# Performance work log

Hardware: AMD Instinct MI355X
Metric: run time of the kernel (lower is better)

The kernel has to match this reference:

```python
import jax, jax.numpy as jnp
import numpy as np

NHEAD, TOKEN_DIM, HIDDEN, OUT_DIM = 4, 768, 256, 768
B, L = 16, 1024
EPS = 1e-5
SLOPE = 0.01  # default LeakyReLU negative_slope


def _layernorm(x, g, b):
    mu = jnp.mean(x, axis=-1, keepdims=True)
    var = jnp.var(x, axis=-1, keepdims=True)
    return (x - mu) * jax.lax.rsqrt(var + EPS) * g + b


def setup_inputs() -> dict:
    key = jax.random.key(0)
    ks = jax.random.split(key, 8)
    s = 0.02
    return {
        "token_embedding": jax.random.normal(ks[0], (B, L, TOKEN_DIM), jnp.float32),
        "W_fc": jax.random.normal(ks[1], (NHEAD, TOKEN_DIM, HIDDEN), jnp.float32) * s,
        "b_fc": jnp.zeros((NHEAD, HIDDEN), jnp.float32),
        "ln_g": jnp.ones((NHEAD, HIDDEN), jnp.float32),
        "ln_b": jnp.zeros((NHEAD, HIDDEN), jnp.float32),
        "a_w": jax.random.normal(ks[2], (NHEAD, 2 * HIDDEN), jnp.float32) * s,
        "a_b": jnp.zeros((NHEAD,), jnp.float32),
        "W_cat": jax.random.normal(ks[3], (NHEAD * HIDDEN, OUT_DIM), jnp.float32) * s,
        "b_cat": jnp.zeros((OUT_DIM,), jnp.float32),
        "lnO_g": jnp.ones((OUT_DIM,), jnp.float32),
        "lnO_b": jnp.zeros((OUT_DIM,), jnp.float32),
        "W_fcs": jax.random.normal(ks[4], (3, OUT_DIM, OUT_DIM), jnp.float32) * s,
        "b_fcs": jnp.zeros((3, OUT_DIM), jnp.float32),
    }


def reference(token_embedding, W_fc, b_fc, ln_g, ln_b, a_w, a_b,
              W_cat, b_cat, lnO_g, lnO_b, W_fcs, b_fcs):
    # per-head projection + layernorm: h [n, B, L, H]
    h = jnp.einsum('bld,ndh->nblh', token_embedding, W_fc) + b_fc[:, None, None, :]
    h = _layernorm(h, ln_g[:, None, None, :], ln_b[:, None, None, :])
    # attn_fc(concat[h_j, h_i]) decomposes linearly:
    # score[n,b,i,j] = a1 . h[n,b,j] + a2 . h[n,b,i] + bias
    s_row = jnp.einsum('nblh,nh->nbl', h, a_w[:, :HIDDEN])   # varies with j
    s_col = jnp.einsum('nblh,nh->nbl', h, a_w[:, HIDDEN:])   # varies with i
    e = s_col[:, :, :, None] + s_row[:, :, None, :] + a_b[:, None, None, None]
    e = jnp.where(e >= 0, e, SLOPE * e)  # LeakyReLU
    attn = jax.nn.softmax(e, axis=-1)    # softmax over j
    h_prime = jnp.einsum('nbij,nbjh->nbih', attn, h)  # [n, B, L, H]
    # concat heads on feature dim -> [B, L, n*H]
    concat_out = jnp.transpose(h_prime, (1, 2, 0, 3)).reshape(B, L, NHEAD * HIDDEN)
    sent = jnp.mean(concat_out, axis=1)  # [B, n*H]
    sent = sent @ W_cat + b_cat
    sent = _layernorm(sent, lnO_g, lnO_b)
    dims_out = [sent @ W_fcs[i] + b_fcs[i] for i in range(3)]
    return (dims_out[0], dims_out[1], dims_out[2], sent)
```

## Files before the change

kernel.cpp:

```cpp
#include <hip/hip_runtime.h>
#include <math.h>


#define NH   4
#define TD   768
#define HID  256
#define OD   768
#define BB   16
#define LL   1024
#define RTOT (BB*LL)
#define L2E  1.4426950408889634f

typedef __attribute__((ext_vector_type(8))) short bf16x8;
typedef __attribute__((ext_vector_type(4))) float f32x4;

#if __has_builtin(__builtin_amdgcn_exp2f)
#define EXP2(x) __builtin_amdgcn_exp2f(x)
#else
#define EXP2(x) __expf((x) * 0.6931471805599453f)
#endif
#if __has_builtin(__builtin_amdgcn_logf)
#define LOG2(x) __builtin_amdgcn_logf(x)
#else
#define LOG2(x) (__logf(x) * L2E)
#endif

__device__ __forceinline__ float lrelu(float x) { return fmaxf(x, 0.01f * x); }

__device__ __forceinline__ float waveReduceSum(float v) {
  #pragma unroll
  for (int m = 1; m < 64; m <<= 1) v += __shfl_xor(v, m, 64);
  return v;
}
__device__ __forceinline__ float waveReduceMax(float v) {
  #pragma unroll
  for (int m = 1; m < 64; m <<= 1) v = fmaxf(v, __shfl_xor(v, m, 64));
  return v;
}
__device__ __forceinline__ float red16(float v) {
  v += __shfl_xor(v, 1, 64); v += __shfl_xor(v, 2, 64);
  v += __shfl_xor(v, 4, 64); v += __shfl_xor(v, 8, 64);
  return v;
}

__device__ __forceinline__ unsigned short f2b(float f) {
  union { float f; unsigned u; } v; v.f = f;
  unsigned u = v.u;
  return (unsigned short)((u + 0x7fffu + ((u >> 16) & 1u)) >> 16);
}
__device__ __forceinline__ float b2f(unsigned short h) {
  union { unsigned u; float f; } v; v.u = ((unsigned)h) << 16;
  return v.f;
}

__device__ __forceinline__ void gll16(const void* g, void* l) {
  __builtin_amdgcn_global_load_lds(
      (const __attribute__((address_space(1))) unsigned int*)g,
      (__attribute__((address_space(3))) unsigned int*)l, 16, 0, 0);
}

__global__ __launch_bounds__(256) void kconv(const float* __restrict__ T,
                                             const float* __restrict__ Wfc,
                                             unsigned short* __restrict__ Tb,
                                             unsigned short* __restrict__ Wtb) {
  __shared__ float tile[64][65];
  const int t = threadIdx.x;
  if (blockIdx.x < 6144) {
    const size_t i = ((size_t)blockIdx.x * 256 + t) * 8;
    const float4 a = *(const float4*)(T + i);
    const float4 b = *(const float4*)(T + i + 4);
    bf16x8 o;
    o[0] = (short)f2b(a.x); o[1] = (short)f2b(a.y);
    o[2] = (short)f2b(a.z); o[3] = (short)f2b(a.w);
    o[4] = (short)f2b(b.x); o[5] = (short)f2b(b.y);
    o[6] = (short)f2b(b.z); o[7] = (short)f2b(b.w);
    *(bf16x8*)(Tb + i) = o;
  } else {
    const int b2 = blockIdx.x - 6144;
    const int ct = b2 & 3;
    const int kt = (b2 >> 2) % 12;
    const int n  = b2 / 48;
    #pragma unroll
    for (int i = 0; i < 16; ++i) {
      const int kl = i * 4 + (t >> 6), cl = t & 63;
      tile[kl][cl] =
          Wfc[(size_t)n * TD * HID + (size_t)(kt * 64 + kl) * HID + ct * 64 + cl];
    }
    __syncthreads();
    #pragma unroll
    for (int i = 0; i < 16; ++i) {
      const int cl = i * 4 + (t >> 6), kl = t & 63;
      Wtb[(size_t)n * HID * TD + (size_t)(ct * 64 + cl) * TD + kt * 64 + kl] =
          f2b(tile[kl][cl]);
    }
  }
}

__global__ __launch_bounds__(512) void k1_mfma(
    const unsigned short* __restrict__ Tb,
    const unsigned short* __restrict__ Wtb,
    const float* __restrict__ bfc, const float* __restrict__ lng,
    const float* __restrict__ lnb, const float* __restrict__ aw,
    unsigned short* __restrict__ hb,
    float* __restrict__ sR, float* __restrict__ sC)
{
  const int n    = blockIdx.x >> 6;
  const int mb   = blockIdx.x & 63;
  const int t    = threadIdx.x;
  const int lane = t & 63;
  const int wq   = __builtin_amdgcn_readfirstlane(t >> 6);
  const int wm   = wq >> 1;
  const int wn   = wq & 1;
  const int cl   = lane & 15;
  const int rg   = lane >> 4;
  const int row0 = mb * 256;

  __shared__ __align__(16) char smem[131072];

  f32x4 acc[4][8];
  #pragma unroll
  for (int mi = 0; mi < 4; ++mi)
    #pragma unroll
    for (int ni = 0; ni < 8; ++ni) acc[mi][ni] = (f32x4){0.f, 0.f, 0.f, 0.f};

  const char* Tg = (const char*)Tb;
  const char* Wg = (const char*)(Wtb + (size_t)n * HID * TD);

  #define STAGE(buf, k0)                                                       \
    do {                                                                       \
      char* base_ = smem + (buf) * 65536;                                      \
      _Pragma("unroll")                                                        \
      for (int i_ = 0; i_ < 4; ++i_) {                                         \
        const int off_ = i_ * 8192 + t * 16;                                   \
        const int r_ = off_ >> 7, kb_ = off_ & 127;                            \
        const int kbs_ = kb_ ^ ((r_ & 7) << 4);                                \
        gll16(Tg + ((size_t)(row0 + r_) * TD + (k0)) * 2 + kbs_, base_ + off_);\
      }                                                                        \
      _Pragma("unroll")                                                        \
      for (int i_ = 0; i_ < 4; ++i_) {                                         \
        const int off_ = i_ * 8192 + t * 16;                                   \
        const int c_ = off_ >> 7, kb_ = off_ & 127;                            \
        const int kbs_ = kb_ ^ ((c_ & 7) << 4);                                \
        gll16(Wg + ((size_t)c_ * TD + (k0)) * 2 + kbs_, base_ + 32768 + off_); \
      }                                                                        \
    } while (0)

  STAGE(0, 0);
  __syncthreads();
  int cur = 0;
  for (int kt = 0; kt < 12; ++kt) {
    if (kt < 11) STAGE(cur ^ 1, (kt + 1) * 64);
    const char* As = smem + cur * 65536;
    const char* Bs = As + 32768;
    #pragma unroll
    for (int ks = 0; ks < 64; ks += 32) {
      bf16x8 av[4], bv[8];
      const int kk2 = (ks + rg * 8) * 2;
      #pragma unroll
      for (int mi = 0; mi < 4; ++mi) {
        const int row = wm * 64 + mi * 16 + cl;
        av[mi] = *(const bf16x8*)(As + row * 128 + (kk2 ^ ((row & 7) << 4)));
      }
      #pragma unroll
      for (int ni = 0; ni < 8; ++ni) {
        const int row = wn * 128 + ni * 16 + cl;
        bv[ni] = *(const bf16x8*)(Bs + row * 128 + (kk2 ^ ((row & 7) << 4)));
      }
      #pragma unroll
      for (int mi = 0; mi < 4; ++mi)
        #pragma unroll
        for (int ni = 0; ni < 8; ++ni)
          acc[mi][ni] = __builtin_amdgcn_mfma_f32_16x16x32_bf16(
              av[mi], bv[ni], acc[mi][ni], 0, 0, 0);
    }
    __syncthreads();
    cur ^= 1;
  }
  #undef STAGE

  unsigned short* hs = (unsigned short*)smem;
  float* redS  = (float*)(smem + 36864);
  float* redS2 = (float*)(smem + 38912);
  float* redP  = (float*)(smem + 40960);
  float* redC  = (float*)(smem + 43008);

  float bfn[8], gvn[8], bvn[8], a1n[8], a2n[8];
  #pragma unroll
  for (int ni = 0; ni < 8; ++ni) {
    const int c = wn * 128 + ni * 16 + cl;
    bfn[ni] = bfc[n * HID + c];
    gvn[ni] = lng[n * HID + c];
    bvn[ni] = lnb[n * HID + c];
    a1n[ni] = aw[n * (2 * HID) + c];
    a2n[ni] = aw[n * (2 * HID) + HID + c];
  }

  #pragma unroll
  for (int mi = 0; mi < 4; ++mi) {
    #pragma unroll
    for (int r = 0; r < 4; ++r) {
      float s = 0.f, s2 = 0.f;
      #pragma unroll
      for (int ni = 0; ni < 8; ++ni) {
        const float x = acc[mi][ni][r] + bfn[ni];
        acc[mi][ni][r] = x;
        s += x; s2 += x * x;
      }
      s = red16(s); s2 = red16(s2);
      if (cl == 0) {
        const int row = wm * 64 + mi * 16 + rg * 4 + r;
        redS [row * 2 + wn] = s;
// ... 23 lines not shown
      pr = red16(pr); pc = red16(pc);
      if (cl == 0) { redP[row * 2 + wn] = pr; redC[row * 2 + wn] = pc; }
    }
  }
  __syncthreads();
  if (t < 256) {
    sR[n * RTOT + row0 + t] = (redP[t * 2] + redP[t * 2 + 1]) * L2E;
    sC[n * RTOT + row0 + t] = (redC[t * 2] + redC[t * 2 + 1]) * L2E;
  }

  unsigned short* hgb = hb + ((size_t)n * RTOT + row0) * HID;
  #pragma unroll
  for (int c = 0; c < 4; ++c) {
    #pragma unroll
    for (int ni = 0; ni < 8; ++ni)
      #pragma unroll
      for (int r = 0; r < 4; ++r) {
        const int lr  = wm * 16 + rg * 4 + r;
        const int col = wn * 128 + ni * 16 + cl;
        hs[lr * 264 + col] = f2b(acc[c][ni][r]);
      }
    __syncthreads();
    #pragma unroll
    for (int i = 0; i < 4; ++i) {
      const int idx = i * 4096 + t * 8;
      const int lr = idx >> 8, cc = idx & 255;
      const int grow = (lr >> 4) * 64 + c * 16 + (lr & 15);
      *(bf16x8*)&hgb[(size_t)grow * HID + cc] = *(const bf16x8*)&hs[lr * 264 + cc];
    }
    __syncthreads();
  }
}

__global__ __launch_bounds__(256) void k2_lse(
    const float* __restrict__ sR, const float* __restrict__ sC,
    const float* __restrict__ ab, float* __restrict__ q)
{
  const int n  = blockIdx.x >> 7;
  const int b  = (blockIdx.x >> 3) & 15;
  const int ic = blockIdx.x & 7;
  const int t  = threadIdx.x;
  const int base = (n * BB + b) * LL;

  __shared__ float rl[LL];
  __shared__ float r01l[LL];
  __shared__ float red[4];

  const float4 r4 = ((const float4*)(sR + base))[t];
  ((float4*)rl)[t] = r4;
  float4 r01;
  r01.x = 0.01f * r4.x; r01.y = 0.01f * r4.y;
  r01.z = 0.01f * r4.z; r01.w = 0.01f * r4.w;
  ((float4*)r01l)[t] = r01;
  float tm = fmaxf(fmaxf(r4.x, r4.y), fmaxf(r4.z, r4.w));
  tm = waveReduceMax(tm);
  if ((t & 63) == 0) red[t >> 6] = tm;
  __syncthreads();
  const float rmax = fmaxf(fmaxf(red[0], red[1]), fmaxf(red[2], red[3]));

  const int i  = ic * 128 + (t >> 1);
  const int jh = t & 1;
  const float ci = sC[base + i] + ab[n] * L2E;
  const float m  = lrelu(ci + rmax);
  const float a1 = ci - m;
  const float a2 = 0.01f * ci - m;
  float z0 = 0.f, z1 = 0.f, z2 = 0.f, z3 = 0.f;
  #pragma unroll 4
  for (int j4 = jh * 128; j4 < jh * 128 + 128; ++j4) {
    const float4 rr = ((const float4*)rl)[j4];
    const float4 r0 = ((const float4*)r01l)[j4];
    z0 += EXP2(fmaxf(a1 + rr.x, a2 + r0.x));
    z1 += EXP2(fmaxf(a1 + rr.y, a2 + r0.y));
    z2 += EXP2(fmaxf(a1 + rr.z, a2 + r0.z));
    z3 += EXP2(fmaxf(a1 + rr.w, a2 + r0.w));
  }
  float z = (z0 + z1) + (z2 + z3);
  z += __shfl_xor(z, 1, 64);
  if (!jh) q[base + i] = m + LOG2(z);
}

__global__ __launch_bounds__(256) void k23_colw(
    const unsigned short* __restrict__ h, const float* __restrict__ sR,
    const float* __restrict__ sC, const float* __restrict__ ab,
    const float* __restrict__ q, float* __restrict__ partial)
{
  const int n  = blockIdx.x >> 7;
  const int b  = (blockIdx.x >> 3) & 15;
  const int jc = blockIdx.x & 7;
  const int t  = threadIdx.x;
  const int base = (n * BB + b) * LL;

  __shared__ float cls1[LL];
  __shared__ float cls2[LL];
  __shared__ float wl[128];
  __shared__ float red2[8][256];

  {
    const float4 c4 = ((const float4*)(sC + base))[t];
    const float4 q4 = ((const float4*)(q + base))[t];
    float4 v1, v2;
    v1.x = c4.x - q4.x; v2.x = 0.01f * c4.x - q4.x;
    v1.y = c4.y - q4.y; v2.y = 0.01f * c4.y - q4.y;
    v1.z = c4.z - q4.z; v2.z = 0.01f * c4.z - q4.z;
    v1.w = c4.w - q4.w; v2.w = 0.01f * c4.w - q4.w;
    ((float4*)cls1)[t] = v1;
    ((float4*)cls2)[t] = v2;
  }
  __syncthreads();

  {
    const int j  = jc * 128 + (t >> 1);
    const int ih = t & 1;
    const float rj  = sR[base + j] + ab[n] * L2E;
    const float r01 = 0.01f * rj;
    float z0 = 0.f, z1 = 0.f, z2 = 0.f, z3 = 0.f;
    #pragma unroll 4
    for (int i4 = ih * 128; i4 < ih * 128 + 128; ++i4) {
      const float4 c1 = ((const float4*)cls1)[i4];
      const float4 c2 = ((const float4*)cls2)[i4];
      z0 += EXP2(fmaxf(c1.x + rj, c2.x + r01));
      z1 += EXP2(fmaxf(c1.y + rj, c2.y + r01));
      z2 += EXP2(fmaxf(c1.z + rj, c2.z + r01));
      z3 += EXP2(fmaxf(c1.w + rj, c2.w + r01));
    }
    float z = (z0 + z1) + (z2 + z3);
    z += __shfl_xor(z, 1, 64);
    if (!ih) wl[t >> 1] = z * (1.f / LL);
  }
  __syncthreads();

  const int jl = t >> 5;
  const int cg = t & 31;
  const unsigned short* hp =
      h + ((size_t)n * RTOT + b * LL + jc * 128) * HID + cg * 8;
  float a0=0,a1=0,a2=0,a3=0,a4=0,a5=0,a6=0,a7=0;
  #pragma unroll 4
  for (int j = jl; j < 128; j += 8) {
    const bf16x8 v = *(const bf16x8*)(hp + (size_t)j * HID);
    const float w = wl[j];
    a0 = fmaf(w, b2f((unsigned short)v[0]), a0);
    a1 = fmaf(w, b2f((unsigned short)v[1]), a1);
    a2 = fmaf(w, b2f((unsigned short)v[2]), a2);
    a3 = fmaf(w, b2f((unsigned short)v[3]), a3);
    a4 = fmaf(w, b2f((unsigned short)v[4]), a4);
    a5 = fmaf(w, b2f((unsigned short)v[5]), a5);
    a6 = fmaf(w, b2f((unsigned short)v[6]), a6);
    a7 = fmaf(w, b2f((unsigned short)v[7]), a7);
  }
  red2[jl][cg*8+0]=a0; red2[jl][cg*8+1]=a1; red2[jl][cg*8+2]=a2; red2[jl][cg*8+3]=a3;
  red2[jl][cg*8+4]=a4; red2[jl][cg*8+5]=a5; red2[jl][cg*8+6]=a6; red2[jl][cg*8+7]=a7;
  __syncthreads();
  float s = 0.f;
  #pragma unroll
  for (int r = 0; r < 8; ++r) s += red2[r][t];
  partial[((n * BB + b) * 8 + jc) * 256 + t] = s;
}

__global__ __launch_bounds__(256) void k4_cat(
    const float* __restrict__ partial, const float* __restrict__ Wcat,
    float* __restrict__ pcat)
{
  const int kc = blockIdx.x / 3;
  const int oc = blockIdx.x % 3;
  const int t  = threadIdx.x;
  __shared__ float s[64][16];
  {
    const int kk = t >> 2, b4 = (t & 3) * 4;
    const int n = kc >> 2;
    const int c = (kc & 3) * 64 + kk;
    #pragma unroll
    for (int bi = 0; bi < 4; ++bi) {
      const int b = b4 + bi;
      const float* pb = partial + (size_t)((n * BB + b) * 8) * 256 + c;
      float v = 0.f;
      #pragma unroll
      for (int j = 0; j < 8; ++j) v += pb[j * 256];
      s[kk][b] = v;
    }
  }
  __syncthreads();
  const int o = oc * 256 + t;
  const float* W = Wcat + (size_t)(kc * 64) * OD + o;
  float acc[BB];
  #pragma unroll
  for (int b = 0; b < BB; ++b) acc[b] = 0.f;
  #pragma unroll 4
  for (int kk = 0; kk < 64; ++kk) {
    const float w = W[(size_t)kk * OD];
    const f32x4 s0 = *(const f32x4*)&s[kk][0];
    const f32x4 s1 = *(const f32x4*)&s[kk][4];
    const f32x4 s2 = *(const f32x4*)&s[kk][8];
    const f32x4 s3 = *(const f32x4*)&s[kk][12];
    acc[0]=fmaf(s0.x,w,acc[0]);  acc[1]=fmaf(s0.y,w,acc[1]);
    acc[2]=fmaf(s0.z,w,acc[2]);  acc[3]=fmaf(s0.w,w,acc[3]);
    acc[4]=fmaf(s1.x,w,acc[4]);  acc[5]=fmaf(s1.y,w,acc[5]);
    acc[6]=fmaf(s1.z,w,acc[6]);  acc[7]=fmaf(s1.w,w,acc[7]);
    acc[8]=fmaf(s2.x,w,acc[8]);  acc[9]=fmaf(s2.y,w,acc[9]);
    acc[10]=fmaf(s2.z,w,acc[10]); acc[11]=fmaf(s2.w,w,acc[11]);
    acc[12]=fmaf(s3.x,w,acc[12]); acc[13]=fmaf(s3.y,w,acc[13]);
    acc[14]=fmaf(s3.z,w,acc[14]); acc[15]=fmaf(s3.w,w,acc[15]);
  }
  float* P = pcat + (size_t)(kc * BB) * OD + o;
  #pragma unroll
  for (int b = 0; b < BB; ++b) P[(size_t)b * OD] = acc[b];
}

__global__ __launch_bounds__(256) void k4_ln(
    const float* __restrict__ pcat, const float* __restrict__ bcat,
    const float* __restrict__ g, const float* __restrict__ be,
    float* __restrict__ sent, float* __restrict__ out_sent)
{
  const int b = blockIdx.x;
  const int t = threadIdx.x;
  __shared__ float red[4][2];
  float x[3];
  #pragma unroll
  for (int i = 0; i < 3; ++i) {
    const int o = i * 256 + t;
    float v = bcat[o];
    #pragma unroll
    for (int kc = 0; kc < 16; ++kc) v += pcat[(size_t)(kc * BB + b) * OD + o];
    x[i] = v;
  }
  float s  = x[0] + x[1] + x[2];
  float s2 = x[0]*x[0] + x[1]*x[1] + x[2]*x[2];
  s = waveReduceSum(s); s2 = waveReduceSum(s2);
  if ((t & 63) == 0) { red[t >> 6][0] = s; red[t >> 6][1] = s2; }
  __syncthreads();
  s  = red[0][0] + red[1][0] + red[2][0] + red[3][0];
  s2 = red[0][1] + red[1][1] + red[2][1] + red[3][1];
  const float mu  = s * (1.f / OD);
  const float var = s2 * (1.f / OD) - mu * mu;
  const float rs  = rsqrtf(var + 1e-5f);
  #pragma unroll
  for (int i = 0; i < 3; ++i) {
    const int o = i * 256 + t;
    const float y = (x[i] - mu) * rs * g[o] + be[o];
    sent[b * OD + o]     = y;
    out_sent[b * OD + o] = y;
  }
}

__global__ __launch_bounds__(256) void k4_fcs(
    const float* __restrict__ sent, const float* __restrict__ Wfcs,
    float* __restrict__ pfcs)
{
  const int kc = blockIdx.x / 9;
  const int r  = blockIdx.x % 9;
  const int i  = r / 3, oc = r % 3;
  const int t  = threadIdx.x;
  __shared__ float s[64][16];
  {
    const int kk = t >> 2, b4 = (t & 3) * 4;
    #pragma unroll
    for (int bi = 0; bi < 4; ++bi)
      s[kk][b4 + bi] = sent[(b4 + bi) * OD + kc * 64 + kk];
  }
  __syncthreads();
  const int o = oc * 256 + t;
  const float* W = Wfcs + (size_t)i * OD * OD + (size_t)(kc * 64) * OD + o;
  float acc[BB];
  #pragma unroll
  for (int b = 0; b < BB; ++b) acc[b] = 0.f;
  #pragma unroll 4
  for (int kk = 0; kk < 64; ++kk) {
    const float w = W[(size_t)kk * OD];
    const f32x4 s0 = *(const f32x4*)&s[kk][0];
    const f32x4 s1 = *(const f32x4*)&s[kk][4];
    const f32x4 s2 = *(const f32x4*)&s[kk][8];
    const f32x4 s3 = *(const f32x4*)&s[kk][12];
    acc[0]=fmaf(s0.x,w,acc[0]);  acc[1]=fmaf(s0.y,w,acc[1]);
    acc[2]=fmaf(s0.z,w,acc[2]);  acc[3]=fmaf(s0.w,w,acc[3]);
    acc[4]=fmaf(s1.x,w,acc[4]);  acc[5]=fmaf(s1.y,w,acc[5]);
    acc[6]=fmaf(s1.z,w,acc[6]);  acc[7]=fmaf(s1.w,w,acc[7]);
    acc[8]=fmaf(s2.x,w,acc[8]);  acc[9]=fmaf(s2.y,w,acc[9]);
    acc[10]=fmaf(s2.z,w,acc[10]); acc[11]=fmaf(s2.w,w,acc[11]);
    acc[12]=fmaf(s3.x,w,acc[12]); acc[13]=fmaf(s3.y,w,acc[13]);
    acc[14]=fmaf(s3.z,w,acc[14]); acc[15]=fmaf(s3.w,w,acc[15]);
  }
  float* P = pfcs + (size_t)((kc * 3 + i) * BB) * OD + o;
  #pragma unroll
  for (int b = 0; b < BB; ++b) P[(size_t)b * OD] = acc[b];
}

__global__ __launch_bounds__(256) void k4_red(
    const float* __restrict__ pfcs, const float* __restrict__ bfcs,
    float* __restrict__ out)
{
  const int i = blockIdx.x >> 4;
  const int b = blockIdx.x & 15;
  const int t = threadIdx.x;
  #pragma unroll
  for (int oc = 0; oc < 3; ++oc) {
    const int o = oc * 256 + t;
    float v = bfcs[i * OD + o];
    #pragma unroll
    for (int kc = 0; kc < 12; ++kc)
      v += pfcs[(size_t)((kc * 3 + i) * BB + b) * OD + o];
    out[i * (BB * OD) + b * OD + o] = v;
  }
}

extern "C" void kernel_launch(void* const* d_in, const int* in_sizes, int n_in,
                              void* d_out, int out_size, void* d_ws, size_t ws_size,
                              hipStream_t stream)
{
  const float* T    = (const float*)d_in[0];
  const float* Wfc  = (const float*)d_in[1];
  const float* bfc  = (const float*)d_in[2];
  const float* lng  = (const float*)d_in[3];
  const float* lnb  = (const float*)d_in[4];
  const float* aw   = (const float*)d_in[5];
  const float* ab   = (const float*)d_in[6];
  const float* Wcat = (const float*)d_in[7];
  const float* bcat = (const float*)d_in[8];
  const float* lnOg = (const float*)d_in[9];
  const float* lnOb = (const float*)d_in[10];
  const float* Wfcs = (const float*)d_in[11];
  const float* bfcs = (const float*)d_in[12];
  float* out = (float*)d_out;

  char* W = (char*)d_ws;
  unsigned short* Tb  = (unsigned short*)W;
  unsigned short* Wtb = (unsigned short*)(W + 25165824);
  unsigned short* hb  = (unsigned short*)(W + 26738688);
  float* sR      = (float*)(W + 60293120);
  float* sC      = sR + NH * RTOT;
  float* q       = sC + NH * RTOT;
  float* partial = q + NH * RTOT;
  float* sent    = partial + NH * BB * 8 * 256;
  float* pcat    = sent + BB * OD;
  float* pfcs    = pcat + 16 * BB * OD;

  kconv   <<<dim3(6336), dim3(256), 0, stream>>>(T, Wfc, Tb, Wtb);
  k1_mfma <<<dim3(256),  dim3(512), 0, stream>>>(Tb, Wtb, bfc, lng, lnb, aw, hb, sR, sC);
  k2_lse  <<<dim3(512),  dim3(256), 0, stream>>>(sR, sC, ab, q);
  k23_colw<<<dim3(512),  dim3(256), 0, stream>>>(hb, sR, sC, ab, q, partial);
  k4_cat  <<<dim3(48),   dim3(256), 0, stream>>>(partial, Wcat, pcat);
  k4_ln   <<<dim3(16),   dim3(256), 0, stream>>>(pcat, bcat, lnOg, lnOb, sent, out + 3 * BB * OD);
  k4_fcs  <<<dim3(108),  dim3(256), 0, stream>>>(sent, Wfcs, pfcs);
  k4_red  <<<dim3(48),   dim3(256), 0, stream>>>(pfcs, bfcs, out);
}
```

Baseline: 104.3 us.

## Fuse fp32-to-bf16 token conversion into GEMM A-tile staging via registers

Result: no change. 103.3 us (median of 2 runs) (-1.0%).

```diff
diff --git a/kernel.cpp b/kernel.cpp
--- a/kernel.cpp
+++ b/kernel.cpp
@@ -52,6 +52,11 @@
   union { unsigned u; float f; } v; v.u = ((unsigned)h) << 16;
   return v.f;
 }
+__device__ __forceinline__ unsigned cvtpk(float lo, float hi) {
+  unsigned r;
+  asm("v_cvt_pk_bf16_f32 %0, %1, %2" : "=v"(r) : "v"(lo), "v"(hi));
+  return r;
+}
 
 __device__ __forceinline__ void gll16(const void* g, void* l) {
   __builtin_amdgcn_global_load_lds(
@@ -59,45 +64,30 @@
       (__attribute__((address_space(3))) unsigned int*)l, 16, 0, 0);
 }
 
-__global__ __launch_bounds__(256) void kconv(const float* __restrict__ T,
-                                             const float* __restrict__ Wfc,
-                                             unsigned short* __restrict__ Tb,
-                                             unsigned short* __restrict__ Wtb) {
+__global__ __launch_bounds__(256) void kconv_w(const float* __restrict__ src,
+                                               unsigned short* __restrict__ dst) {
   __shared__ float tile[64][65];
-  const int t = threadIdx.x;
-  if (blockIdx.x < 6144) {
-    const size_t i = ((size_t)blockIdx.x * 256 + t) * 8;
-    const float4 a = *(const float4*)(T + i);
-    const float4 b = *(const float4*)(T + i + 4);
-    bf16x8 o;
-    o[0] = (short)f2b(a.x); o[1] = (short)f2b(a.y);
-    o[2] = (short)f2b(a.z); o[3] = (short)f2b(a.w);
-    o[4] = (short)f2b(b.x); o[5] = (short)f2b(b.y);
-    o[6] = (short)f2b(b.z); o[7] = (short)f2b(b.w);
-    *(bf16x8*)(Tb + i) = o;
-  } else {
-    const int b2 = blockIdx.x - 6144;
-    const int ct = b2 & 3;
-    const int kt = (b2 >> 2) % 12;
-    const int n  = b2 / 48;
-    #pragma unroll
-    for (int i = 0; i < 16; ++i) {
-      const int kl = i * 4 + (t >> 6), cl = t & 63;
-      tile[kl][cl] =
-          Wfc[(size_t)n * TD * HID + (size_t)(kt * 64 + kl) * HID + ct * 64 + cl];
-    }
-    __syncthreads();
-    #pragma unroll
-    for (int i = 0; i < 16; ++i) {
-      const int cl = i * 4 + (t >> 6), kl = t & 63;
-      Wtb[(size_t)n * HID * TD + (size_t)(ct * 64 + cl) * TD + kt * 64 + kl] =
-          f2b(tile[kl][cl]);
-    }
+  const int t  = threadIdx.x;
+  const int ct = blockIdx.x & 3;
+  const int kt = (blockIdx.x >> 2) % 12;
+  const int n  = blockIdx.x / 48;
+  #pragma unroll
+  for (int i = 0; i < 16; ++i) {
+    const int kl = i * 4 + (t >> 6), cl = t & 63;
+    tile[kl][cl] =
+        src[(size_t)n * TD * HID + (size_t)(kt * 64 + kl) * HID + ct * 64 + cl];
+  }
+  __syncthreads();
+  #pragma unroll
+  for (int i = 0; i < 16; ++i) {
+    const int cl = i * 4 + (t >> 6), kl = t & 63;
+    dst[(size_t)n * HID * TD + (size_t)(ct * 64 + cl) * TD + kt * 64 + kl] =
+        f2b(tile[kl][cl]);
   }
 }
 
 __global__ __launch_bounds__(512) void k1_mfma(
-    const unsigned short* __restrict__ Tb,
+    const float* __restrict__ T,
     const unsigned short* __restrict__ Wtb,
     const float* __restrict__ bfc, const float* __restrict__ lng,
     const float* __restrict__ lnb, const float* __restrict__ aw,
@@ -123,33 +113,61 @@
     #pragma unroll
     for (int ni = 0; ni < 8; ++ni) acc[mi][ni] = (f32x4){0.f, 0.f, 0.f, 0.f};
 
-  const char* Tg = (const char*)Tb;
   const char* Wg = (const char*)(Wtb + (size_t)n * HID * TD);
 
-  #define STAGE(buf, k0)                                                       \
+  #define LDA(r, k0)                                                           \
     do {                                                                       \
-      char* base_ = smem + (buf) * 65536;                                      \
       _Pragma("unroll")                                                        \
-      for (int i_ = 0; i_ < 4; ++i_) {                                         \
-        const int off_ = i_ * 8192 + t * 16;                                   \
-        const int r_ = off_ >> 7, kb_ = off_ & 127;                            \
-        const int kbs_ = kb_ ^ ((r_ & 7) << 4);                                \
-        gll16(Tg + ((size_t)(row0 + r_) * TD + (k0)) * 2 + kbs_, base_ + off_);\
+      for (int j_ = 0; j_ < 4; ++j_) {                                         \
+        const float* p_ = T + (size_t)(row0 + j_ * 64 + (t >> 3)) * TD +       \
+                          (k0) + (t & 7) * 8;                                  \
+        r[2 * j_]     = *(const float4*)p_;                                    \
+        r[2 * j_ + 1] = *(const float4*)(p_ + 4);                              \
       }                                                                        \
+    } while (0)
+
+  #define WRA(buf, r)                                                          \
+    do {                                                                       \
+      char* ab_ = smem + (buf) * 65536;                                        \
+      _Pragma("unroll")                                                        \
+      for (int j_ = 0; j_ < 4; ++j_) {                                         \
+        const int row_ = j_ * 64 + (t >> 3);                                   \
+        const int kb_  = (t & 7) * 16;                                         \
+        uint4 p_;                                                              \
+        p_.x = cvtpk(r[2 * j_].x,     r[2 * j_].y);                            \
+        p_.y = cvtpk(r[2 * j_].z,     r[2 * j_].w);                            \
+        p_.z = cvtpk(r[2 * j_ + 1].x, r[2 * j_ + 1].y);                        \
+        p_.w = cvtpk(r[2 * j_ + 1].z, r[2 * j_ + 1].w);                        \
+        *(uint4*)(ab_ + row_ * 128 + (kb_ ^ ((row_ & 7) << 4))) = p_;          \
+      }                                                                        \
+    } while (0)
+
+  #define STAGE_B(buf, k0)                                                     \
+    do {                                                                       \
+      char* bb_ = smem + (buf) * 65536 + 32768;                                \
       _Pragma("unroll")                                                        \
       for (int i_ = 0; i_ < 4; ++i_) {                                         \
         const int off_ = i_ * 8192 + t * 16;                                   \
         const int c_ = off_ >> 7, kb_ = off_ & 127;                            \
         const int kbs_ = kb_ ^ ((c_ & 7) << 4);                                \
-        gll16(Wg + ((size_t)c_ * TD + (k0)) * 2 + kbs_, base_ + 32768 + off_); \
+        gll16(Wg + ((size_t)c_ * TD + (k0)) * 2 + kbs_, bb_ + off_);           \
       }                                                                        \
     } while (0)
 
-  STAGE(0, 0);
-  __syncthreads();
+  float4 rA[8];
+  LDA(rA, 0);
+  STAGE_B(0, 0);
+  WRA(0, rA);
+  LDA(rA, 64);
+  __syncthreads();
+
   int cur = 0;
   for (int kt = 0; kt < 12; ++kt) {
-    if (kt < 11) STAGE(cur ^ 1, (kt + 1) * 64);
+    if (kt < 11) {
+      STAGE_B(cur ^ 1, (kt + 1) * 64);
+      WRA(cur ^ 1, rA);
+      if (kt < 10) LDA(rA, (kt + 2) * 64);
+    }
     const char* As = smem + cur * 65536;
     const char* Bs = As + 32768;
     #pragma unroll
@@ -176,7 +194,9 @@
     __syncthreads();
     cur ^= 1;
   }
-  #undef STAGE
+  #undef LDA
+  #undef WRA
+  #undef STAGE_B
 
   unsigned short* hs = (unsigned short*)smem;
   float* redS  = (float*)(smem + 36864);
@@ -555,10 +575,9 @@
   float* out = (float*)d_out;
 
   char* W = (char*)d_ws;
-  unsigned short* Tb  = (unsigned short*)W;
-  unsigned short* Wtb = (unsigned short*)(W + 25165824);
-  unsigned short* hb  = (unsigned short*)(W + 26738688);
-  float* sR      = (float*)(W + 60293120);
+  unsigned short* Wtb = (unsigned short*)W;
+  unsigned short* hb  = (unsigned short*)(W + 1572864);
+  float* sR      = (float*)(W + 35127296);
   float* sC      = sR + NH * RTOT;
   float* q       = sC + NH * RTOT;
   float* partial = q + NH * RTOT;
@@ -566,8 +585,8 @@
   float* pcat    = sent + BB * OD;
   float* pfcs    = pcat + 16 * BB * OD;
 
-  kconv   <<<dim3(6336), dim3(256), 0, stream>>>(T, Wfc, Tb, Wtb);
-  k1_mfma <<<dim3(256),  dim3(512), 0, stream>>>(Tb, Wtb, bfc, lng, lnb, aw, hb, sR, sC);
+  kconv_w <<<dim3(192),  dim3(256), 0, stream>>>(Wfc, Wtb);
+  k1_mfma <<<dim3(256),  dim3(512), 0, stream>>>(T, Wtb, bfc, lng, lnb, aw, hb, sR, sC);
   k2_lse  <<<dim3(512),  dim3(256), 0, stream>>>(sR, sC, ab, q);
   k23_colw<<<dim3(512),  dim3(256), 0, stream>>>(hb, sR, sC, ab, q, partial);
   k4_cat  <<<dim3(48),   dim3(256), 0, stream>>>(partial, Wcat, pcat);
```

## Triple-buffer projection GEMM with K=32 stages and manual vmcnt barriers

Applied to the files above, without the earlier changes.

New measurement: 105.1 us. Within noise of the previous version (+0.8%).

```diff
diff --git a/kernel.cpp b/kernel.cpp
--- a/kernel.cpp
+++ b/kernel.cpp
@@ -115,7 +115,7 @@
   const int rg   = lane >> 4;
   const int row0 = mb * 256;
 
-  __shared__ __align__(16) char smem[131072];
+  __shared__ __align__(16) char smem[98304];
 
   f32x4 acc[4][8];
   #pragma unroll
@@ -128,55 +128,76 @@
 
   #define STAGE(buf, k0)                                                       \
     do {                                                                       \
-      char* base_ = smem + (buf) * 65536;                                      \
+      char* base_ = smem + (buf) * 32768;                                      \
       _Pragma("unroll")                                                        \
-      for (int i_ = 0; i_ < 4; ++i_) {                                         \
+      for (int i_ = 0; i_ < 2; ++i_) {                                         \
         const int off_ = i_ * 8192 + t * 16;                                   \
-        const int r_ = off_ >> 7, kb_ = off_ & 127;                            \
-        const int kbs_ = kb_ ^ ((r_ & 7) << 4);                                \
+        const int r_ = off_ >> 6, kb_ = off_ & 63;                             \
+        const int kbs_ = kb_ ^ (((r_ >> 1) & 3) << 4);                         \
         gll16(Tg + ((size_t)(row0 + r_) * TD + (k0)) * 2 + kbs_, base_ + off_);\
       }                                                                        \
       _Pragma("unroll")                                                        \
-      for (int i_ = 0; i_ < 4; ++i_) {                                         \
+      for (int i_ = 0; i_ < 2; ++i_) {                                         \
         const int off_ = i_ * 8192 + t * 16;                                   \
-        const int c_ = off_ >> 7, kb_ = off_ & 127;                            \
-        const int kbs_ = kb_ ^ ((c_ & 7) << 4);                                \
-        gll16(Wg + ((size_t)c_ * TD + (k0)) * 2 + kbs_, base_ + 32768 + off_); \
+        const int c_ = off_ >> 6, kb_ = off_ & 63;                             \
+        const int kbs_ = kb_ ^ (((c_ >> 1) & 3) << 4);                         \
+        gll16(Wg + ((size_t)c_ * TD + (k0)) * 2 + kbs_,                        \
+              base_ + 16384 + off_);                                           \
       }                                                                        \
     } while (0)
 
+  #define COMPUTE(buf)                                                         \
+    do {                                                                       \
+      const char* As_ = smem + (buf) * 32768;                                  \
+      const char* Bs_ = As_ + 16384;                                           \
+      bf16x8 av_[4], bv_[8];                                                   \
+      const int kk2_ = rg * 16;                                                \
+      _Pragma("unroll")                                                        \
+      for (int mi = 0; mi < 4; ++mi) {                                         \
+        const int row_ = wm * 64 + mi * 16 + cl;                               \
+        av_[mi] = *(const bf16x8*)(As_ + row_ * 64 +                           \
+                                   (kk2_ ^ (((row_ >> 1) & 3) << 4)));         \
+      }                                                                        \
+      _Pragma("unroll")                                                        \
+      for (int ni = 0; ni < 8; ++ni) {                                         \
+        const int row_ = wn * 128 + ni * 16 + cl;                              \
+        bv_[ni] = *(const bf16x8*)(Bs_ + row_ * 64 +                           \
+                                   (kk2_ ^ (((row_ >> 1) & 3) << 4)));         \
+      }                                                                        \
+      _Pragma("unroll")                                                        \
+      for (int mi = 0; mi < 4; ++mi)                                           \
+        _Pragma("unroll")                                                      \
+        for (int ni = 0; ni < 8; ++ni)                                         \
+          acc[mi][ni] = __builtin_amdgcn_mfma_f32_16x16x32_bf16(               \
+              av_[mi], bv_[ni], acc[mi][ni], 0, 0, 0);                         \
+    } while (0)
+
+  #define BODY(BC, BP, kt)                                                     \
+    do {                                                                       \
+      if ((kt) < 22) STAGE(BP, ((kt) + 2) * 32);                               \
+      COMPUTE(BC);                                                             \
+      if ((kt) < 22)       asm volatile("s_waitcnt vmcnt(4)" ::: "memory");    \
+      else if ((kt) == 22) asm volatile("s_waitcnt vmcnt(0)" ::: "memory");    \
+      if ((kt) < 23) asm volatile("s_barrier" ::: "memory");                   \
+    } while (0)
+
   STAGE(0, 0);
-  __syncthreads();
-  int cur = 0;
-  for (int kt = 0; kt < 12; ++kt) {
-    if (kt < 11) STAGE(cur ^ 1, (kt + 1) * 64);
-    const char* As = smem + cur * 65536;
-    const char* Bs = As + 32768;
-    #pragma unroll
-    for (int ks = 0; ks < 64; ks += 32) {
-      bf16x8 av[4], bv[8];
-      const int kk2 = (ks + rg * 8) * 2;
-      #pragma unroll
-      for (int mi = 0; mi < 4; ++mi) {
-        const int row = wm * 64 + mi * 16 + cl;
-        av[mi] = *(const bf16x8*)(As + row * 128 + (kk2 ^ ((row & 7) << 4)));
-      }
-      #pragma unroll
-      for (int ni = 0; ni < 8; ++ni) {
-        const int row = wn * 128 + ni * 16 + cl;
-        bv[ni] = *(const bf16x8*)(Bs + row * 128 + (kk2 ^ ((row & 7) << 4)));
-      }
-      #pragma unroll
-      for (int mi = 0; mi < 4; ++mi)
-        #pragma unroll
-        for (int ni = 0; ni < 8; ++ni)
-          acc[mi][ni] = __builtin_amdgcn_mfma_f32_16x16x32_bf16(
-              av[mi], bv[ni], acc[mi][ni], 0, 0, 0);
-    }
-    __syncthreads();
-    cur ^= 1;
+  STAGE(1, 32);
+  asm volatile("s_waitcnt vmcnt(4)" ::: "memory");
+  asm volatile("s_barrier" ::: "memory");
+
+  #pragma unroll 1
+  for (int k3 = 0; k3 < 8; ++k3) {
+    const int kt = k3 * 3;
+    BODY(0, 2, kt);
+    BODY(1, 0, kt + 1);
+    BODY(2, 1, kt + 2);
   }
   #undef STAGE
+  #undef COMPUTE
+  #undef BODY
+
+  __syncthreads();
 
   unsigned short* hs = (unsigned short*)smem;
   float* redS  = (float*)(smem + 36864);
```

## Fuse six tail kernels into one cooperative kernel with grid syncs

Applied to the files above, without the earlier changes.

After: 340.5 us. +226.5%, slower.

```diff
diff --git a/kernel.cpp b/kernel.cpp
--- a/kernel.cpp
+++ b/kernel.cpp
@@ -1,6 +1,9 @@
 #include <hip/hip_runtime.h>
+#include <hip/hip_cooperative_groups.h>
 #include <math.h>
 
+
+namespace cg = cooperative_groups;
 
 #define NH   4
 #define TD   768
@@ -266,272 +269,268 @@
   }
 }
 
-__global__ __launch_bounds__(256) void k2_lse(
-    const float* __restrict__ sR, const float* __restrict__ sC,
-    const float* __restrict__ ab, float* __restrict__ q)
-{
-  const int n  = blockIdx.x >> 7;
-  const int b  = (blockIdx.x >> 3) & 15;
-  const int ic = blockIdx.x & 7;
-  const int t  = threadIdx.x;
-  const int base = (n * BB + b) * LL;
-
-  __shared__ float rl[LL];
-  __shared__ float r01l[LL];
-  __shared__ float red[4];
-
-  const float4 r4 = ((const float4*)(sR + base))[t];
-  ((float4*)rl)[t] = r4;
-  float4 r01;
-  r01.x = 0.01f * r4.x; r01.y = 0.01f * r4.y;
-  r01.z = 0.01f * r4.z; r01.w = 0.01f * r4.w;
-  ((float4*)r01l)[t] = r01;
-  float tm = fmaxf(fmaxf(r4.x, r4.y), fmaxf(r4.z, r4.w));
-  tm = waveReduceMax(tm);
-  if ((t & 63) == 0) red[t >> 6] = tm;
-  __syncthreads();
-  const float rmax = fmaxf(fmaxf(red[0], red[1]), fmaxf(red[2], red[3]));
-
-  const int i  = ic * 128 + (t >> 1);
-  const int jh = t & 1;
-  const float ci = sC[base + i] + ab[n] * L2E;
-  const float m  = lrelu(ci + rmax);
-  const float a1 = ci - m;
-  const float a2 = 0.01f * ci - m;
-  float z0 = 0.f, z1 = 0.f, z2 = 0.f, z3 = 0.f;
-  #pragma unroll 4
-  for (int j4 = jh * 128; j4 < jh * 128 + 128; ++j4) {
-    const float4 rr = ((const float4*)rl)[j4];
-    const float4 r0 = ((const float4*)r01l)[j4];
-    z0 += EXP2(fmaxf(a1 + rr.x, a2 + r0.x));
-    z1 += EXP2(fmaxf(a1 + rr.y, a2 + r0.y));
-    z2 += EXP2(fmaxf(a1 + rr.z, a2 + r0.z));
-    z3 += EXP2(fmaxf(a1 + rr.w, a2 + r0.w));
-  }
-  float z = (z0 + z1) + (z2 + z3);
-  z += __shfl_xor(z, 1, 64);
-  if (!jh) q[base + i] = m + LOG2(z);
-}
-
-__global__ __launch_bounds__(256) void k23_colw(
+__global__ __launch_bounds__(256) void k_tail(
     const unsigned short* __restrict__ h, const float* __restrict__ sR,
     const float* __restrict__ sC, const float* __restrict__ ab,
-    const float* __restrict__ q, float* __restrict__ partial)
+    float* __restrict__ q, float* __restrict__ partial,
+    const float* __restrict__ Wcat, float* __restrict__ pcat,
+    const float* __restrict__ bcat, const float* __restrict__ lnOg,
+    const float* __restrict__ lnOb, float* __restrict__ sent,
+    float* __restrict__ out_sent, const float* __restrict__ Wfcs,
+    float* __restrict__ pfcs, const float* __restrict__ bfcs,
+    float* __restrict__ out)
 {
-  const int n  = blockIdx.x >> 7;
-  const int b  = (blockIdx.x >> 3) & 15;
-  const int jc = blockIdx.x & 7;
-  const int t  = threadIdx.x;
-  const int base = (n * BB + b) * LL;
-
-  __shared__ float cls1[LL];
-  __shared__ float cls2[LL];
-  __shared__ float wl[128];
-  __shared__ float red2[8][256];
+  cg::grid_group grid = cg::this_grid();
+  __shared__ __align__(16) char sm[17408];
+  const int bid = blockIdx.x;
+  const int t   = threadIdx.x;
 
   {
-    const float4 c4 = ((const float4*)(sC + base))[t];
-    const float4 q4 = ((const float4*)(q + base))[t];
-    float4 v1, v2;
-    v1.x = c4.x - q4.x; v2.x = 0.01f * c4.x - q4.x;
-    v1.y = c4.y - q4.y; v2.y = 0.01f * c4.y - q4.y;
-    v1.z = c4.z - q4.z; v2.z = 0.01f * c4.z - q4.z;
-    v1.w = c4.w - q4.w; v2.w = 0.01f * c4.w - q4.w;
-    ((float4*)cls1)[t] = v1;
-    ((float4*)cls2)[t] = v2;
-  }
-  __syncthreads();
-
-  {
-    const int j  = jc * 128 + (t >> 1);
-    const int ih = t & 1;
-    const float rj  = sR[base + j] + ab[n] * L2E;
-    const float r01 = 0.01f * rj;
+    float* rl   = (float*)sm;
+    float* r01l = rl + 1024;
+    float* red  = r01l + 1024;
+    const int n  = bid >> 7;
+    const int b  = (bid >> 3) & 15;
+    const int ic = bid & 7;
+    const int base = (n * BB + b) * LL;
+
+    const float4 r4 = ((const float4*)(sR + base))[t];
+    ((float4*)rl)[t] = r4;
+    float4 r01;
+    r01.x = 0.01f * r4.x; r01.y = 0.01f * r4.y;
+    r01.z = 0.01f * r4.z; r01.w = 0.01f * r4.w;
+    ((float4*)r01l)[t] = r01;
+    float tm = fmaxf(fmaxf(r4.x, r4.y), fmaxf(r4.z, r4.w));
+    tm = waveReduceMax(tm);
+    if ((t & 63) == 0) red[t >> 6] = tm;
+    __syncthreads();
+    const float rmax = fmaxf(fmaxf(red[0], red[1]), fmaxf(red[2], red[3]));
+
+    const int i  = ic * 128 + (t >> 1);
+    const int jh = t & 1;
+    const float ci = sC[base + i] + ab[n] * L2E;
+    const float m  = lrelu(ci + rmax);
+    const float a1 = ci - m;
+    const float a2 = 0.01f * ci - m;
     float z0 = 0.f, z1 = 0.f, z2 = 0.f, z3 = 0.f;
     #pragma unroll 4
-    for (int i4 = ih * 128; i4 < ih * 128 + 128; ++i4) {
-      const float4 c1 = ((const float4*)cls1)[i4];
-      const float4 c2 = ((const float4*)cls2)[i4];
-      z0 += EXP2(fmaxf(c1.x + rj, c2.x + r01));
-      z1 += EXP2(fmaxf(c1.y + rj, c2.y + r01));
-      z2 += EXP2(fmaxf(c1.z + rj, c2.z + r01));
-      z3 += EXP2(fmaxf(c1.w + rj, c2.w + r01));
+    for (int j4 = jh * 128; j4 < jh * 128 + 128; ++j4) {
+      const float4 rr = ((const float4*)rl)[j4];
+      const float4 r0 = ((const float4*)r01l)[j4];
+      z0 += EXP2(fmaxf(a1 + rr.x, a2 + r0.x));
+      z1 += EXP2(fmaxf(a1 + rr.y, a2 + r0.y));
+      z2 += EXP2(fmaxf(a1 + rr.z, a2 + r0.z));
+      z3 += EXP2(fmaxf(a1 + rr.w, a2 + r0.w));
     }
     float z = (z0 + z1) + (z2 + z3);
     z += __shfl_xor(z, 1, 64);
-    if (!ih) wl[t >> 1] = z * (1.f / LL);
-  }
-  __syncthreads();
-
-  const int jl = t >> 5;
-  const int cg = t & 31;
-  const unsigned short* hp =
-      h + ((size_t)n * RTOT + b * LL + jc * 128) * HID + cg * 8;
-  float a0=0,a1=0,a2=0,a3=0,a4=0,a5=0,a6=0,a7=0;
-  #pragma unroll 4
-  for (int j = jl; j < 128; j += 8) {
-    const bf16x8 v = *(const bf16x8*)(hp + (size_t)j * HID);
-    const float w = wl[j];
-    a0 = fmaf(w, b2f((unsigned short)v[0]), a0);
-    a1 = fmaf(w, b2f((unsigned short)v[1]), a1);
-    a2 = fmaf(w, b2f((unsigned short)v[2]), a2);
-    a3 = fmaf(w, b2f((unsigned short)v[3]), a3);
-    a4 = fmaf(w, b2f((unsigned short)v[4]), a4);
-    a5 = fmaf(w, b2f((unsigned short)v[5]), a5);
-    a6 = fmaf(w, b2f((unsigned short)v[6]), a6);
-    a7 = fmaf(w, b2f((unsigned short)v[7]), a7);
-  }
-  red2[jl][cg*8+0]=a0; red2[jl][cg*8+1]=a1; red2[jl][cg*8+2]=a2; red2[jl][cg*8+3]=a3;
-  red2[jl][cg*8+4]=a4; red2[jl][cg*8+5]=a5; red2[jl][cg*8+6]=a6; red2[jl][cg*8+7]=a7;
-  __syncthreads();
-  float s = 0.f;
-  #pragma unroll
-  for (int r = 0; r < 8; ++r) s += red2[r][t];
-  partial[((n * BB + b) * 8 + jc) * 256 + t] = s;
-}
-
-__global__ __launch_bounds__(256) void k4_cat(
-    const float* __restrict__ partial, const float* __restrict__ Wcat,
-    float* __restrict__ pcat)
-{
-  const int kc = blockIdx.x / 3;
-  const int oc = blockIdx.x % 3;
-  const int t  = threadIdx.x;
-  __shared__ float s[64][16];
+    if (!jh) q[base + i] = m + LOG2(z);
+  }
+  grid.sync();
+
   {
-    const int kk = t >> 2, b4 = (t & 3) * 4;
-    const int n = kc >> 2;
-    const int c = (kc & 3) * 64 + kk;
-    #pragma unroll
-    for (int bi = 0; bi < 4; ++bi) {
-      const int b = b4 + bi;
-      const float* pb = partial + (size_t)((n * BB + b) * 8) * 256 + c;
-      float v = 0.f;
-      #pragma unroll
-      for (int j = 0; j < 8; ++j) v += pb[j * 256];
-      s[kk][b] = v;
-    }
-  }
-  __syncthreads();
-  const int o = oc * 256 + t;
-  const float* W = Wcat + (size_t)(kc * 64) * OD + o;
-  float acc[BB];
-  #pragma unroll
-  for (int b = 0; b < BB; ++b) acc[b] = 0.f;
-  #pragma unroll 4
-  for (int kk = 0; kk < 64; ++kk) {
-    const float w = W[(size_t)kk * OD];
-    const f32x4 s0 = *(const f32x4*)&s[kk][0];
-    const f32x4 s1 = *(const f32x4*)&s[kk][4];
-    const f32x4 s2 = *(const f32x4*)&s[kk][8];
-    const f32x4 s3 = *(const f32x4*)&s[kk][12];
-    acc[0]=fmaf(s0.x,w,acc[0]);  acc[1]=fmaf(s0.y,w,acc[1]);
-    acc[2]=fmaf(s0.z,w,acc[2]);  acc[3]=fmaf(s0.w,w,acc[3]);
-    acc[4]=fmaf(s1.x,w,acc[4]);  acc[5]=fmaf(s1.y,w,acc[5]);
-    acc[6]=fmaf(s1.z,w,acc[6]);  acc[7]=fmaf(s1.w,w,acc[7]);
-    acc[8]=fmaf(s2.x,w,acc[8]);  acc[9]=fmaf(s2.y,w,acc[9]);
-    acc[10]=fmaf(s2.z,w,acc[10]); acc[11]=fmaf(s2.w,w,acc[11]);
-    acc[12]=fmaf(s3.x,w,acc[12]); acc[13]=fmaf(s3.y,w,acc[13]);
-    acc[14]=fmaf(s3.z,w,acc[14]); acc[15]=fmaf(s3.w,w,acc[15]);
-  }
-  float* P = pcat + (size_t)(kc * BB) * OD + o;
-  #pragma unroll
-  for (int b = 0; b < BB; ++b) P[(size_t)b * OD] = acc[b];
-}
-
-__global__ __launch_bounds__(256) void k4_ln(
-    const float* __restrict__ pcat, const float* __restrict__ bcat,
-    const float* __restrict__ g, const float* __restrict__ be,
-    float* __restrict__ sent, float* __restrict__ out_sent)
-{
-  const int b = blockIdx.x;
-  const int t = threadIdx.x;
-  __shared__ float red[4][2];
-  float x[3];
-  #pragma unroll
-  for (int i = 0; i < 3; ++i) {
-    const int o = i * 256 + t;
-    float v = bcat[o];
-    #pragma unroll
-    for (int kc = 0; kc < 16; ++kc) v += pcat[(size_t)(kc * BB + b) * OD + o];
-    x[i] = v;
-  }
-  float s  = x[0] + x[1] + x[2];
-  float s2 = x[0]*x[0] + x[1]*x[1] + x[2]*x[2];
-  s = waveReduceSum(s); s2 = waveReduceSum(s2);
-  if ((t & 63) == 0) { red[t >> 6][0] = s; red[t >> 6][1] = s2; }
-  __syncthreads();
-  s  = red[0][0] + red[1][0] + red[2][0] + red[3][0];
-  s2 = red[0][1] + red[1][1] + red[2][1] + red[3][1];
-  const float mu  = s * (1.f / OD);
-  const float var = s2 * (1.f / OD) - mu * mu;
-  const float rs  = rsqrtf(var + 1e-5f);
-  #pragma unroll
-  for (int i = 0; i < 3; ++i) {
-    const int o = i * 256 + t;
-    const float y = (x[i] - mu) * rs * g[o] + be[o];
-    sent[b * OD + o]     = y;
-    out_sent[b * OD + o] = y;
-  }
-}
-
-__global__ __launch_bounds__(256) void k4_fcs(
-    const float* __restrict__ sent, const float* __restrict__ Wfcs,
-    float* __restrict__ pfcs)
-{
-  const int kc = blockIdx.x / 9;
-  const int r  = blockIdx.x % 9;
-  const int i  = r / 3, oc = r % 3;
-  const int t  = threadIdx.x;
-  __shared__ float s[64][16];
-  {
-    const int kk = t >> 2, b4 = (t & 3) * 4;
-    #pragma unroll
-    for (int bi = 0; bi < 4; ++bi)
-      s[kk][b4 + bi] = sent[(b4 + bi) * OD + kc * 64 + kk];
-  }
-  __syncthreads();
-  const int o = oc * 256 + t;
-  const float* W = Wfcs + (size_t)i * OD * OD + (size_t)(kc * 64) * OD + o;
-  float acc[BB];
-  #pragma unroll
-  for (int b = 0; b < BB; ++b) acc[b] = 0.f;
-  #pragma unroll 4
-  for (int kk = 0; kk < 64; ++kk) {
-    const float w = W[(size_t)kk * OD];
-    const f32x4 s0 = *(const f32x4*)&s[kk][0];
-    const f32x4 s1 = *(const f32x4*)&s[kk][4];
-    const f32x4 s2 = *(const f32x4*)&s[kk][8];
-    const f32x4 s3 = *(const f32x4*)&s[kk][12];
-    acc[0]=fmaf(s0.x,w,acc[0]);  acc[1]=fmaf(s0.y,w,acc[1]);
-    acc[2]=fmaf(s0.z,w,acc[2]);  acc[3]=fmaf(s0.w,w,acc[3]);
-    acc[4]=fmaf(s1.x,w,acc[4]);  acc[5]=fmaf(s1.y,w,acc[5]);
-    acc[6]=fmaf(s1.z,w,acc[6]);  acc[7]=fmaf(s1.w,w,acc[7]);
-    acc[8]=fmaf(s2.x,w,acc[8]);  acc[9]=fmaf(s2.y,w,acc[9]);
-    acc[10]=fmaf(s2.z,w,acc[10]); acc[11]=fmaf(s2.w,w,acc[11]);
-    acc[12]=fmaf(s3.x,w,acc[12]); acc[13]=fmaf(s3.y,w,acc[13]);
-    acc[14]=fmaf(s3.z,w,acc[14]); acc[15]=fmaf(s3.w,w,acc[15]);
-  }
-  float* P = pfcs + (size_t)((kc * 3 + i) * BB) * OD + o;
-  #pragma unroll
-  for (int b = 0; b < BB; ++b) P[(size_t)b * OD] = acc[b];
-}
-
-__global__ __launch_bounds__(256) void k4_red(
-    const float* __restrict__ pfcs, const float* __restrict__ bfcs,
-    float* __restrict__ out)
-{
-  const int i = blockIdx.x >> 4;
-  const int b = blockIdx.x & 15;
-  const int t = threadIdx.x;
-  #pragma unroll
-  for (int oc = 0; oc < 3; ++oc) {
+    float* cls1 = (float*)sm;
+    float* cls2 = cls1 + 1024;
+    float* wl   = cls2 + 1024;
+    float* red2 = wl + 128;
+    const int n  = bid >> 7;
+    const int b  = (bid >> 3) & 15;
+    const int jc = bid & 7;
+    const int base = (n * BB + b) * LL;
+
+    {
+      const float4 c4 = ((const float4*)(sC + base))[t];
+      const float4 q4 = ((const float4*)(q + base))[t];
+      float4 v1, v2;
+      v1.x = c4.x - q4.x; v2.x = 0.01f * c4.x - q4.x;
+      v1.y = c4.y - q4.y; v2.y = 0.01f * c4.y - q4.y;
+      v1.z = c4.z - q4.z; v2.z = 0.01f * c4.z - q4.z;
+      v1.w = c4.w - q4.w; v2.w = 0.01f * c4.w - q4.w;
+      ((float4*)cls1)[t] = v1;
+      ((float4*)cls2)[t] = v2;
+    }
+    __syncthreads();
+
+    {
+      const int j  = jc * 128 + (t >> 1);
+      const int ih = t & 1;
+      const float rj  = sR[base + j] + ab[n] * L2E;
+      const float r01 = 0.01f * rj;
+      float z0 = 0.f, z1 = 0.f, z2 = 0.f, z3 = 0.f;
+      #pragma unroll 4
+      for (int i4 = ih * 128; i4 < ih * 128 + 128; ++i4) {
+        const float4 c1 = ((const float4*)cls1)[i4];
+        const float4 c2 = ((const float4*)cls2)[i4];
+        z0 += EXP2(fmaxf(c1.x + rj, c2.x + r01));
+        z1 += EXP2(fmaxf(c1.y + rj, c2.y + r01));
+        z2 += EXP2(fmaxf(c1.z + rj, c2.z + r01));
+        z3 += EXP2(fmaxf(c1.w + rj, c2.w + r01));
+      }
+      float z = (z0 + z1) + (z2 + z3);
+      z += __shfl_xor(z, 1, 64);
+      if (!ih) wl[t >> 1] = z * (1.f / LL);
+    }
+    __syncthreads();
+
+    const int jl = t >> 5;
+    const int cg2 = t & 31;
+    const unsigned short* hp =
+        h + ((size_t)n * RTOT + b * LL + jc * 128) * HID + cg2 * 8;
+    float a0=0,a1=0,a2=0,a3=0,a4=0,a5=0,a6=0,a7=0;
+    #pragma unroll 4
+    for (int j = jl; j < 128; j += 8) {
+      const bf16x8 v = *(const bf16x8*)(hp + (size_t)j * HID);
+      const float w = wl[j];
+      a0 = fmaf(w, b2f((unsigned short)v[0]), a0);
+      a1 = fmaf(w, b2f((unsigned short)v[1]), a1);
+      a2 = fmaf(w, b2f((unsigned short)v[2]), a2);
+      a3 = fmaf(w, b2f((unsigned short)v[3]), a3);
+      a4 = fmaf(w, b2f((unsigned short)v[4]), a4);
+      a5 = fmaf(w, b2f((unsigned short)v[5]), a5);
+      a6 = fmaf(w, b2f((unsigned short)v[6]), a6);
+      a7 = fmaf(w, b2f((unsigned short)v[7]), a7);
+    }
+    red2[jl*256 + cg2*8+0]=a0; red2[jl*256 + cg2*8+1]=a1;
+    red2[jl*256 + cg2*8+2]=a2; red2[jl*256 + cg2*8+3]=a3;
+    red2[jl*256 + cg2*8+4]=a4; red2[jl*256 + cg2*8+5]=a5;
+    red2[jl*256 + cg2*8+6]=a6; red2[jl*256 + cg2*8+7]=a7;
+    __syncthreads();
+    float s = 0.f;
+    #pragma unroll
+    for (int r = 0; r < 8; ++r) s += red2[r*256 + t];
+    partial[((n * BB + b) * 8 + jc) * 256 + t] = s;
+  }
+  grid.sync();
+
+  if (bid < 48) {
+    float* s = (float*)sm;
+    const int kc = bid / 3;
+    const int oc = bid % 3;
+    {
+      const int kk = t >> 2, b4 = (t & 3) * 4;
+      const int n = kc >> 2;
+      const int c = (kc & 3) * 64 + kk;
+      #pragma unroll
+      for (int bi = 0; bi < 4; ++bi) {
+        const int b = b4 + bi;
+        const float* pb = partial + (size_t)((n * BB + b) * 8) * 256 + c;
+        float v = 0.f;
+        #pragma unroll
+        for (int j = 0; j < 8; ++j) v += pb[j * 256];
+        s[kk * 16 + b] = v;
+      }
+    }
+    __syncthreads();
     const int o = oc * 256 + t;
-    float v = bfcs[i * OD + o];
-    #pragma unroll
-    for (int kc = 0; kc < 12; ++kc)
-      v += pfcs[(size_t)((kc * 3 + i) * BB + b) * OD + o];
-    out[i * (BB * OD) + b * OD + o] = v;
+    const float* W = Wcat + (size_t)(kc * 64) * OD + o;
+    float acc[BB];
+    #pragma unroll
+    for (int b = 0; b < BB; ++b) acc[b] = 0.f;
+    #pragma unroll 4
+    for (int kk = 0; kk < 64; ++kk) {
+      const float w = W[(size_t)kk * OD];
+      const f32x4 s0 = *(const f32x4*)&s[kk * 16 + 0];
+      const f32x4 s1 = *(const f32x4*)&s[kk * 16 + 4];
+      const f32x4 s2 = *(const f32x4*)&s[kk * 16 + 8];
+      const f32x4 s3 = *(const f32x4*)&s[kk * 16 + 12];
+      acc[0]=fmaf(s0.x,w,acc[0]);  acc[1]=fmaf(s0.y,w,acc[1]);
+      acc[2]=fmaf(s0.z,w,acc[2]);  acc[3]=fmaf(s0.w,w,acc[3]);
+      acc[4]=fmaf(s1.x,w,acc[4]);  acc[5]=fmaf(s1.y,w,acc[5]);
+      acc[6]=fmaf(s1.z,w,acc[6]);  acc[7]=fmaf(s1.w,w,acc[7]);
+      acc[8]=fmaf(s2.x,w,acc[8]);  acc[9]=fmaf(s2.y,w,acc[9]);
+      acc[10]=fmaf(s2.z,w,acc[10]); acc[11]=fmaf(s2.w,w,acc[11]);
+      acc[12]=fmaf(s3.x,w,acc[12]); acc[13]=fmaf(s3.y,w,acc[13]);
+      acc[14]=fmaf(s3.z,w,acc[14]); acc[15]=fmaf(s3.w,w,acc[15]);
+    }
+    float* P = pcat + (size_t)(kc * BB) * OD + o;
+    #pragma unroll
+    for (int b = 0; b < BB; ++b) P[(size_t)b * OD] = acc[b];
+  }
+  grid.sync();
+
+  if (bid < 16) {
+    float* red = (float*)sm;
+    const int b = bid;
+    float x[3];
+    #pragma unroll
+    for (int i = 0; i < 3; ++i) {
+      const int o = i * 256 + t;
+      float v = bcat[o];
+      #pragma unroll
+      for (int kc = 0; kc < 16; ++kc) v += pcat[(size_t)(kc * BB + b) * OD + o];
+      x[i] = v;
+    }
+    float s  = x[0] + x[1] + x[2];
+    float s2 = x[0]*x[0] + x[1]*x[1] + x[2]*x[2];
+    s = waveReduceSum(s); s2 = waveReduceSum(s2);
+    if ((t & 63) == 0) { red[(t >> 6) * 2] = s; red[(t >> 6) * 2 + 1] = s2; }
+    __syncthreads();
+    s  = red[0] + red[2] + red[4] + red[6];
+    s2 = red[1] + red[3] + red[5] + red[7];
+    const float mu  = s * (1.f / OD);
+    const float var = s2 * (1.f / OD) - mu * mu;
+    const float rs  = rsqrtf(var + 1e-5f);
+    #pragma unroll
+    for (int i = 0; i < 3; ++i) {
+      const int o = i * 256 + t;
+      const float y = (x[i] - mu) * rs * lnOg[o] + lnOb[o];
+      sent[b * OD + o]     = y;
+      out_sent[b * OD + o] = y;
+    }
+  }
+  grid.sync();
+
+  if (bid < 108) {
+    float* s = (float*)sm;
+    const int kc = bid / 9;
+    const int r  = bid % 9;
+    const int i  = r / 3, oc = r % 3;
+    {
+      const int kk = t >> 2, b4 = (t & 3) * 4;
+      #pragma unroll
+      for (int bi = 0; bi < 4; ++bi)
+        s[kk * 16 + b4 + bi] = sent[(b4 + bi) * OD + kc * 64 + kk];
+    }
+    __syncthreads();
+    const int o = oc * 256 + t;
+    const float* W = Wfcs + (size_t)i * OD * OD + (size_t)(kc * 64) * OD + o;
+    float acc[BB];
+    #pragma unroll
+    for (int b = 0; b < BB; ++b) acc[b] = 0.f;
+    #pragma unroll 4
+    for (int kk = 0; kk < 64; ++kk) {
+      const float w = W[(size_t)kk * OD];
+      const f32x4 s0 = *(const f32x4*)&s[kk * 16 + 0];
+      const f32x4 s1 = *(const f32x4*)&s[kk * 16 + 4];
+      const f32x4 s2 = *(const f32x4*)&s[kk * 16 + 8];
+      const f32x4 s3 = *(const f32x4*)&s[kk * 16 + 12];
+      acc[0]=fmaf(s0.x,w,acc[0]);  acc[1]=fmaf(s0.y,w,acc[1]);
+      acc[2]=fmaf(s0.z,w,acc[2]);  acc[3]=fmaf(s0.w,w,acc[3]);
+      acc[4]=fmaf(s1.x,w,acc[4]);  acc[5]=fmaf(s1.y,w,acc[5]);
+      acc[6]=fmaf(s1.z,w,acc[6]);  acc[7]=fmaf(s1.w,w,acc[7]);
+      acc[8]=fmaf(s2.x,w,acc[8]);  acc[9]=fmaf(s2.y,w,acc[9]);
+      acc[10]=fmaf(s2.z,w,acc[10]); acc[11]=fmaf(s2.w,w,acc[11]);
+      acc[12]=fmaf(s3.x,w,acc[12]); acc[13]=fmaf(s3.y,w,acc[13]);
+      acc[14]=fmaf(s3.z,w,acc[14]); acc[15]=fmaf(s3.w,w,acc[15]);
+    }
+    float* P = pfcs + (size_t)((kc * 3 + i) * BB) * OD + o;
+    #pragma unroll
+    for (int b = 0; b < BB; ++b) P[(size_t)b * OD] = acc[b];
+  }
+  grid.sync();
+
+  if (bid < 48) {
+    const int i = bid >> 4;
+    const int b = bid & 15;
+    #pragma unroll
+    for (int oc = 0; oc < 3; ++oc) {
+      const int o = oc * 256 + t;
+      float v = bfcs[i * OD + o];
+      #pragma unroll
+      for (int kc = 0; kc < 12; ++kc)
+        v += pfcs[(size_t)((kc * 3 + i) * BB + b) * OD + o];
+      out[i * (BB * OD) + b * OD + o] = v;
+    }
   }
 }
 
@@ -565,13 +564,17 @@
   float* sent    = partial + NH * BB * 8 * 256;
   float* pcat    = sent + BB * OD;
   float* pfcs    = pcat + 16 * BB * OD;
+  float* out_sent = out + 3 * BB * OD;
 
   kconv   <<<dim3(6336), dim3(256), 0, stream>>>(T, Wfc, Tb, Wtb);
   k1_mfma <<<dim3(256),  dim3(512), 0, stream>>>(Tb, Wtb, bfc, lng, lnb, aw, hb, sR, sC);
-  k2_lse  <<<dim3(512),  dim3(256), 0, stream>>>(sR, sC, ab, q);
-  k23_colw<<<dim3(512),  dim3(256), 0, stream>>>(hb, sR, sC, ab, q, partial);
-  k4_cat  <<<dim3(48),   dim3(256), 0, stream>>>(partial, Wcat, pcat);
-  k4_ln   <<<dim3(16),   dim3(256), 0, stream>>>(pcat, bcat, lnOg, lnOb, sent, out + 3 * BB * OD);
-  k4_fcs  <<<dim3(108),  dim3(256), 0, stream>>>(sent, Wfcs, pfcs);
-  k4_red  <<<dim3(48),   dim3(256), 0, stream>>>(pfcs, bfcs, out);
-}
+
+  void* args[] = {
+    (void*)&hb, (void*)&sR, (void*)&sC, (void*)&ab, (void*)&q, (void*)&partial,
+    (void*)&Wcat, (void*)&pcat, (void*)&bcat, (void*)&lnOg, (void*)&lnOb,
+    (void*)&sent, (void*)&out_sent, (void*)&Wfcs, (void*)&pfcs, (void*)&bfcs,
+    (void*)&out
+  };
+  hipLaunchCooperativeKernel((const void*)k_tail, dim3(512), dim3(256),
+                             args, 0, stream);
+}
```
